# Kernel optimization log

Measured on AMD Instinct MI355X. Metric: run time of the kernel, lower is better.

The kernel has to match this reference:

```python
import jax, jax.numpy as jnp
import numpy as np

EMB = 1024
HEADS = 16
HD = EMB // HEADS

def setup_inputs() -> dict:
    key = jax.random.key(0)
    ks = jax.random.split(key, 9)
    s = 1.0 / np.sqrt(EMB)
    x = jax.random.normal(ks[0], (4, 2048, EMB), dtype=jnp.float32)
    Wq = jax.random.uniform(ks[1], (EMB, EMB), jnp.float32, -s, s)
    bq = jax.random.uniform(ks[2], (EMB,), jnp.float32, -s, s)
    Wk = jax.random.uniform(ks[3], (EMB, EMB), jnp.float32, -s, s)
    bk = jax.random.uniform(ks[4], (EMB,), jnp.float32, -s, s)
    Wv = jax.random.uniform(ks[5], (EMB, EMB), jnp.float32, -s, s)
    bv = jax.random.uniform(ks[6], (EMB,), jnp.float32, -s, s)
    Wo = jax.random.uniform(ks[7], (EMB, EMB), jnp.float32, -s, s)
    bo = jax.random.uniform(ks[8], (EMB,), jnp.float32, -s, s)
    return {"x": x, "Wq": Wq, "bq": bq, "Wk": Wk, "bk": bk, "Wv": Wv, "bv": bv, "Wo": Wo, "bo": bo}

def reference(x, Wq, bq, Wk, bk, Wv, bv, Wo, bo):
    B, T, C = x.shape
    # projections (torch Linear: y = x @ W^T + b)
    q = (x @ Wq.T + bq).reshape(B, T, HEADS, HD).transpose(0, 2, 1, 3)  # [B,H,T,hd]
    k = (x @ Wk.T + bk).reshape(B, T, HEADS, HD).transpose(0, 2, 1, 3)
    v = (x @ Wv.T + bv).reshape(B, T, HEADS, HD).transpose(0, 2, 1, 3)
    scores = jnp.einsum('bhqd,bhkd->bhqk', q, k) / jnp.sqrt(jnp.float32(HD))
    weights = jax.nn.softmax(scores, axis=-1)
    attn = jnp.einsum('bhqk,bhkd->bhqd', weights, v)
    out = attn.transpose(0, 2, 1, 3).reshape(B, T, C)
    return out @ Wo.T + bo
```

## Files before the change

kernel.cpp:

```cpp
#include <hip/hip_runtime.h>

#define TSEQ  2048
#define BATCH 4
#define NHEAD 16
#define EMB   1024

typedef __attribute__((ext_vector_type(8))) __bf16 bf16x8;
typedef __attribute__((ext_vector_type(4))) __bf16 bf16x4;
typedef __attribute__((ext_vector_type(4))) float  floatx4;
typedef __attribute__((ext_vector_type(2))) unsigned int uint32x2;
typedef __attribute__((ext_vector_type(4))) unsigned int uint32x4;

__device__ __forceinline__ void gload_lds16(const __bf16* g, __bf16* lds_uniform_base) {
  __builtin_amdgcn_global_load_lds(
      (__attribute__((address_space(1))) void*)(g),
      (__attribute__((address_space(3))) void*)(lds_uniform_base),
      16, 0, 0);
}

__global__ __launch_bounds__(256) void cvt_f32_bf16(
    const float* __restrict__ src, __bf16* __restrict__ dst)
{
  const int gid = (blockIdx.x * 256 + threadIdx.x) * 4;
  const float4 v = *(const float4*)(src + gid);
  dst[gid + 0] = (__bf16)v.x;
  dst[gid + 1] = (__bf16)v.y;
  dst[gid + 2] = (__bf16)v.z;
  dst[gid + 3] = (__bf16)v.w;
}

__global__ __launch_bounds__(256) void cvt_w4(
    const float* __restrict__ s0, const float* __restrict__ s1,
    const float* __restrict__ s2, const float* __restrict__ s3,
    __bf16* __restrict__ d0, __bf16* __restrict__ d1,
    __bf16* __restrict__ d2, __bf16* __restrict__ d3)
{
  const int z = blockIdx.z;
  const float* src = (z == 0) ? s0 : (z == 1) ? s1 : (z == 2) ? s2 : s3;
  __bf16*      dst = (z == 0) ? d0 : (z == 1) ? d1 : (z == 2) ? d2 : d3;
  const int gid = (blockIdx.x * 256 + threadIdx.x) * 4;
  const float4 v = *(const float4*)(src + gid);
  dst[gid + 0] = (__bf16)v.x;
  dst[gid + 1] = (__bf16)v.y;
  dst[gid + 2] = (__bf16)v.z;
  dst[gid + 3] = (__bf16)v.w;
}

__global__ __launch_bounds__(256) void gemm_bt_bias(
    const __bf16* __restrict__ A,
    const __bf16* __restrict__ W0, const __bf16* __restrict__ W1, const __bf16* __restrict__ W2,
    const float* __restrict__ B0, const float* __restrict__ B1, const float* __restrict__ B2,
    __bf16* __restrict__ C0, __bf16* __restrict__ C1, __bf16* __restrict__ C2)
{
  const int z = blockIdx.z;
  const __bf16* W  = (z == 0) ? W0 : ((z == 1) ? W1 : W2);
  const float*  Bb = (z == 0) ? B0 : ((z == 1) ? B1 : B2);
  __bf16*       C  = (z == 0) ? C0 : ((z == 1) ? C1 : C2);
  const float  scl = (z == 0) ? 0.125f * 1.44269504088896340736f : 1.0f;

  const int tid  = threadIdx.x;
  const int lane = tid & 63;
  const int wid  = tid >> 6;
  const int l16  = lane & 15;
  const int quad = lane >> 4;
  const int wm   = wid & 1;
  const int wn   = wid >> 1;
  const int lin = blockIdx.x + blockIdx.y * 8;
  const int swz = (lin & 7) * 64 + (lin >> 3);
  const int m0  = (swz >> 3) * 128;
  const int n0  = (swz & 7) * 128;

  __shared__ alignas(16) __bf16 As[128 * 32];
  __shared__ alignas(16) __bf16 Bs[128 * 32];

  floatx4 acc[4][4];
#pragma unroll
  for (int i = 0; i < 4; i++)
#pragma unroll
    for (int j = 0; j < 4; j++) acc[i][j] = (floatx4){0.f, 0.f, 0.f, 0.f};

  const int srow = tid >> 2;
  const int sseg = tid & 3;

  for (int k0 = 0; k0 < 1024; k0 += 32) {
    __syncthreads();
#pragma unroll
    for (int is = 0; is < 2; is++) {
      const int row = is * 64 + srow;
      gload_lds16(A + (size_t)(m0 + row) * 1024 + k0 + sseg * 8,
                  &As[(is * 256 + wid * 64) * 8]);
      gload_lds16(W + (size_t)(n0 + row) * 1024 + k0 + sseg * 8,
                  &Bs[(is * 256 + wid * 64) * 8]);
    }
    __syncthreads();

    bf16x8 af[4], bfr[4];
#pragma unroll
    for (int i = 0; i < 4; i++) {
      af[i]  = *(const bf16x8*)(&As[(wm * 64 + i * 16 + l16) * 32 + quad * 8]);
      bfr[i] = *(const bf16x8*)(&Bs[(wn * 64 + i * 16 + l16) * 32 + quad * 8]);
    }
#pragma unroll
    for (int i = 0; i < 4; i++)
#pragma unroll
      for (int j = 0; j < 4; j++)
        acc[i][j] = __builtin_amdgcn_mfma_f32_16x16x32_bf16(af[i], bfr[j], acc[i][j], 0, 0, 0);
  }

  float bv[4];
#pragma unroll
  for (int j = 0; j < 4; j++) bv[j] = Bb[n0 + wn * 64 + j * 16 + l16];

#pragma unroll
  for (int i = 0; i < 4; i++) {
    const size_t mrow = (size_t)m0 + wm * 64 + i * 16 + quad * 4;
#pragma unroll
    for (int j = 0; j < 4; j++) {
      const int col = n0 + wn * 64 + j * 16 + l16;
#pragma unroll
      for (int r = 0; r < 4; r++)
        C[(mrow + r) * 1024 + col] = (__bf16)((acc[i][j][r] + bv[j]) * scl);
    }
  }
}

__global__ __launch_bounds__(256) void gemm_bt_bias_f32(
    const __bf16* __restrict__ A, const __bf16* __restrict__ W,
    const float* __restrict__ Bb, float* __restrict__ C)
{
  const int tid  = threadIdx.x;
  const int lane = tid & 63;
  const int wid  = tid >> 6;
  const int l16  = lane & 15;
  const int quad = lane >> 4;
  const int wm   = wid & 1;
  const int wn   = wid >> 1;
  const int lin = blockIdx.x + blockIdx.y * 8;
  const int swz = (lin & 7) * 64 + (lin >> 3);
  const int m0  = (swz >> 3) * 128;
  const int n0  = (swz & 7) * 128;

  __shared__ alignas(16) __bf16 As[128 * 32];
  __shared__ alignas(16) __bf16 Bs[128 * 32];

  floatx4 acc[4][4];
#pragma unroll
  for (int i = 0; i < 4; i++)
#pragma unroll
    for (int j = 0; j < 4; j++) acc[i][j] = (floatx4){0.f, 0.f, 0.f, 0.f};

  const int srow = tid >> 2;
  const int sseg = tid & 3;

  for (int k0 = 0; k0 < 1024; k0 += 32) {
    __syncthreads();
#pragma unroll
    for (int is = 0; is < 2; is++) {
      const int row = is * 64 + srow;
      gload_lds16(A + (size_t)(m0 + row) * 1024 + k0 + sseg * 8,
                  &As[(is * 256 + wid * 64) * 8]);
      gload_lds16(W + (size_t)(n0 + row) * 1024 + k0 + sseg * 8,
                  &Bs[(is * 256 + wid * 64) * 8]);
    }
    __syncthreads();

    bf16x8 af[4], bfr[4];
#pragma unroll
    for (int i = 0; i < 4; i++) {
      af[i]  = *(const bf16x8*)(&As[(wm * 64 + i * 16 + l16) * 32 + quad * 8]);
      bfr[i] = *(const bf16x8*)(&Bs[(wn * 64 + i * 16 + l16) * 32 + quad * 8]);
    }
#pragma unroll
    for (int i = 0; i < 4; i++)
#pragma unroll
      for (int j = 0; j < 4; j++)
        acc[i][j] = __builtin_amdgcn_mfma_f32_16x16x32_bf16(af[i], bfr[j], acc[i][j], 0, 0, 0);
  }

  float bv[4];
#pragma unroll
  for (int j = 0; j < 4; j++) bv[j] = Bb[n0 + wn * 64 + j * 16 + l16];

#pragma unroll
  for (int i = 0; i < 4; i++) {
    const size_t mrow = (size_t)m0 + wm * 64 + i * 16 + quad * 4;
#pragma unroll
    for (int j = 0; j < 4; j++) {
      const int col = n0 + wn * 64 + j * 16 + l16;
#pragma unroll
      for (int r = 0; r < 4; r++)
        C[(mrow + r) * 1024 + col] = acc[i][j][r] + bv[j];
    }
  }
}

__global__ __launch_bounds__(256) void v_transpose(
    const __bf16* __restrict__ V, __bf16* __restrict__ VT)
{
  const int t0 = blockIdx.x * 64;
  const int bh = blockIdx.y;
  const int b  = bh >> 4;
  const int h  = bh & 15;
  const int tid = threadIdx.x;

  __shared__ alignas(16) __bf16 Ls[64 * 72];

  const int row = tid >> 2, seg = tid & 3;
  const __bf16* src = V + ((size_t)(b * TSEQ + t0 + row)) * EMB + h * 64;
  *(bf16x8*)(&Ls[row * 72 + seg * 8])       = *(const bf16x8*)(src + seg * 8);
  *(bf16x8*)(&Ls[row * 72 + (seg + 4) * 8]) = *(const bf16x8*)(src + (seg + 4) * 8);
  __syncthreads();

  const int od = tid >> 2, oseg = tid & 3;
  bf16x8 o0, o1;
#pragma unroll
  for (int j = 0; j < 8; j++) o0[j] = Ls[(oseg * 16 + j) * 72 + od];
#pragma unroll
  for (int j = 0; j < 8; j++) o1[j] = Ls[(oseg * 16 + 8 + j) * 72 + od];
  __bf16* dst = VT + ((size_t)bh * 64 + od) * TSEQ + t0 + oseg * 16;
  *(bf16x8*)(dst)     = o0;
  *(bf16x8*)(dst + 8) = o1;
}

#define KVB 64
#define NT  (TSEQ / KVB)

#define FA_STEP(BUF, KT)                                                                  \
  {                                                                                       \
    if ((KT) + 1 < NT) {                                                                  \
      *(bf16x8*)(&Ks[(BUF) ^ 1][soff])            = kv0;                                  \
      *(bf16x8*)(&Ks[(BUF) ^ 1][soff + 32 * 72])  = kv1;                                  \
      *(bf16x8*)(&VTs[(BUF) ^ 1][soff])           = vv0;                                  \
      *(bf16x8*)(&VTs[(BUF) ^ 1][soff + 32 * 72]) = vv1;                                  \
    }                                                                                     \
    if ((KT) + 2 < NT) {                                                                  \
      kv0 = *(const bf16x8*)(ksrc + (size_t)(((KT) + 2) * KVB) * EMB);                    \
      kv1 = *(const bf16x8*)(ksrc + (size_t)(((KT) + 2) * KVB + 32) * EMB);               \
      vv0 = *(const bf16x8*)(vsrc + ((KT) + 2) * KVB);                                    \
      vv1 = *(const bf16x8*)(vsrc + (size_t)32 * TSEQ + ((KT) + 2) * KVB);                \
    }                                                                                     \
    __builtin_amdgcn_s_setprio(1);                                                        \
    bf16x8 pfrag[2][2];                                                                   \
    _Pragma("unroll")                                                                     \
    for (int ks = 0; ks < 2; ks++) {                                                      \
      const bf16x8 ka0 = *(const bf16x8*)(&Ks[BUF][((2 * ks) * 16 + l16) * 72 + quad * 8]);      \
      const bf16x8 ka1 = *(const bf16x8*)(&Ks[BUF][((2 * ks) * 16 + l16) * 72 + 32 + quad * 8]); \
      const bf16x8 kb0 = *(const bf16x8*)(&Ks[BUF][((2 * ks + 1) * 16 + l16) * 72 + quad * 8]);  \
      const bf16x8 kb1 = *(const bf16x8*)(&Ks[BUF][((2 * ks + 1) * 16 + l16) * 72 + 32 + quad * 8]); \
      _Pragma("unroll")                                                                   \
      for (int g = 0; g < 2; g++) {                                                       \
        floatx4 ta = (floatx4){0.f, 0.f, 0.f, 0.f};                                       \
        floatx4 tb = (floatx4){0.f, 0.f, 0.f, 0.f};                                       \
        ta = __builtin_amdgcn_mfma_f32_16x16x32_bf16(ka0, qf[g][0], ta, 0, 0, 0);         \
        ta = __builtin_amdgcn_mfma_f32_16x16x32_bf16(ka1, qf[g][1], ta, 0, 0, 0);         \
        tb = __builtin_amdgcn_mfma_f32_16x16x32_bf16(kb0, qf[g][0], tb, 0, 0, 0);         \
        tb = __builtin_amdgcn_mfma_f32_16x16x32_bf16(kb1, qf[g][1], tb, 0, 0, 0);         \
        bf16x4 pa, pb;                                                                    \
        _Pragma("unroll")                                                                 \
        for (int r = 0; r < 4; r++) pa[r] = (__bf16)__builtin_amdgcn_exp2f(ta[r]);        \
        _Pragma("unroll")                                                                 \
        for (int r = 0; r < 4; r++) pb[r] = (__bf16)__builtin_amdgcn_exp2f(tb[r]);        \
        const uint32x2 A2 = __builtin_bit_cast(uint32x2, pa);                             \
        const uint32x2 B2 = __builtin_bit_cast(uint32x2, pb);                             \
        const uint32x2 r0 = __builtin_amdgcn_permlane32_swap(A2.x, B2.x, false, false);   \
        const uint32x2 r1 = __builtin_amdgcn_permlane32_swap(A2.y, B2.y, false, false);   \
        const uint32x2 s0 = __builtin_amdgcn_permlane16_swap(r0.x, r0.y, false, false);   \
        const uint32x2 s1 = __builtin_amdgcn_permlane16_swap(r1.x, r1.y, false, false);   \
        const uint32x4 fw = (uint32x4){s0.x, s1.x, s0.y, s1.y};                           \
        pfrag[g][ks] = __builtin_bit_cast(bf16x8, fw);                                    \
      }                                                                                   \
    }                                                                                     \
    _Pragma("unroll")                                                                     \
    for (int g = 0; g < 2; g++) {                                                         \
      lacc[g] = __builtin_amdgcn_mfma_f32_16x16x32_bf16(ones, pfrag[g][0], lacc[g], 0, 0, 0); \
      lacc[g] = __builtin_amdgcn_mfma_f32_16x16x32_bf16(ones, pfrag[g][1], lacc[g], 0, 0, 0); \
    }                                                                                     \
    _Pragma("unroll")                                                                     \
    for (int dg = 0; dg < 4; dg++) {                                                      \
      _Pragma("unroll")                                                                   \
      for (int ks = 0; ks < 2; ks++) {                                                    \
        const bf16x8 vf = *(const bf16x8*)(&VTs[BUF][(dg * 16 + l16) * 72 + ks * 32 + quad * 8]); \
        _Pragma("unroll")                                                                 \
        for (int g = 0; g < 2; g++)                                                       \
          Oacc[g][dg] = __builtin_amdgcn_mfma_f32_16x16x32_bf16(vf, pfrag[g][ks], Oacc[g][dg], 0, 0, 0); \
      }                                                                                   \
    }                                                                                     \
    __builtin_amdgcn_s_setprio(0);                                                        \
    __syncthreads();                                                                      \
  }

__global__ __launch_bounds__(256, 4) void flash_attn(
    const __bf16* __restrict__ Q, const __bf16* __restrict__ K,
    const __bf16* __restrict__ VT, __bf16* __restrict__ O)
{
  const int lin = blockIdx.x + blockIdx.y * 16;
  const int swz = (lin & 7) * 128 + (lin >> 3);
  const int qt  = swz & 15;
  const int bh  = swz >> 4;
  const int b    = bh >> 4;
  const int h    = bh & 15;
  const int tid  = threadIdx.x;
  const int wid  = tid >> 6;
  const int lane = tid & 63;
  const int l16  = lane & 15;
  const int quad = lane >> 4;

  __shared__ alignas(16) __bf16 Ks[2][KVB * 72];
  __shared__ alignas(16) __bf16 VTs[2][64 * 72];

  const size_t base = ((size_t)b * TSEQ) * EMB + (size_t)h * 64;
  const __bf16* qptr  = Q + base;
  const __bf16* kptr  = K + base;
  const __bf16* vtptr = VT + (size_t)bh * 64 * TSEQ;
  __bf16*       optr  = O + base;

  const int qb = qt * 128 + wid * 32;

  bf16x8 qf[2][2];
#pragma unroll
  for (int g = 0; g < 2; g++)
#pragma unroll
    for (int hf = 0; hf < 2; hf++)
      qf[g][hf] = *(const bf16x8*)(qptr + (size_t)(qb + g * 16 + l16) * EMB + hf * 32 + quad * 8);

  floatx4 Oacc[2][4];
#pragma unroll
  for (int g = 0; g < 2; g++)
#pragma unroll
    for (int dg = 0; dg < 4; dg++) Oacc[g][dg] = (floatx4){0.f, 0.f, 0.f, 0.f};
  floatx4 lacc[2];
#pragma unroll
  for (int g = 0; g < 2; g++) lacc[g] = (floatx4){0.f, 0.f, 0.f, 0.f};

  const uint32x4 onesw = (uint32x4){0x3F803F80u, 0x3F803F80u, 0x3F803F80u, 0x3F803F80u};
  const bf16x8 ones = __builtin_bit_cast(bf16x8, onesw);

  const int srow = tid >> 3, sseg = tid & 7;
  const __bf16* ksrc = kptr  + (size_t)srow * EMB  + sseg * 8;
  const __bf16* vsrc = vtptr + (size_t)srow * TSEQ + sseg * 8;
  const int soff = srow * 72 + sseg * 8;

  bf16x8 kv0 = *(const bf16x8*)(ksrc);
  bf16x8 kv1 = *(const bf16x8*)(ksrc + (size_t)32 * EMB);
  bf16x8 vv0 = *(const bf16x8*)(vsrc);
  bf16x8 vv1 = *(const bf16x8*)(vsrc + (size_t)32 * TSEQ);
  *(bf16x8*)(&Ks[0][soff])            = kv0;
  *(bf16x8*)(&Ks[0][soff + 32 * 72])  = kv1;
  *(bf16x8*)(&VTs[0][soff])           = vv0;
  *(bf16x8*)(&VTs[0][soff + 32 * 72]) = vv1;
  kv0 = *(const bf16x8*)(ksrc + (size_t)KVB * EMB);
  kv1 = *(const bf16x8*)(ksrc + (size_t)(KVB + 32) * EMB);
  vv0 = *(const bf16x8*)(vsrc + KVB);
  vv1 = *(const bf16x8*)(vsrc + (size_t)32 * TSEQ + KVB);
  __syncthreads();

#pragma unroll 1
  for (int kt = 0; kt < NT; kt += 2) {
    FA_STEP(0, kt);
    FA_STEP(1, kt + 1);
  }

#pragma unroll
  for (int g = 0; g < 2; g++) {
    const float inv = 1.0f / lacc[g][0];
#pragma unroll
    for (int dg = 0; dg < 4; dg++) {
      bf16x4 ov;
#pragma unroll
      for (int r = 0; r < 4; r++) ov[r] = (__bf16)(Oacc[g][dg][r] * inv);
      *(bf16x4*)(optr + (size_t)(qb + g * 16 + l16) * EMB + dg * 16 + quad * 4) = ov;
    }
  }
}

extern "C" void kernel_launch(void* const* d_in, const int* in_sizes, int n_in,
                              void* d_out, int out_size, void* d_ws, size_t ws_size,
                              hipStream_t stream) {
  const float* x  = (const float*)d_in[0];
  const float* Wq = (const float*)d_in[1];
  const float* bq = (const float*)d_in[2];
  const float* Wk = (const float*)d_in[3];
  const float* bk = (const float*)d_in[4];
  const float* Wv = (const float*)d_in[5];
  const float* bv = (const float*)d_in[6];
  const float* Wo = (const float*)d_in[7];
  const float* bo = (const float*)d_in[8];
  float* out = (float*)d_out;

  const size_t NELEM = (size_t)BATCH * TSEQ * EMB;
  const size_t WELEM = (size_t)EMB * EMB;

  __bf16* q_b  = (__bf16*)d_out;
  __bf16* k_b  = q_b + NELEM;
  __bf16* x_b  = (__bf16*)d_ws;
  __bf16* v_b  = x_b + NELEM;
  __bf16* wq_b = v_b + NELEM;
  __bf16* wk_b = wq_b + WELEM;
  __bf16* wv_b = wk_b + WELEM;
  __bf16* wo_b = wv_b + WELEM;

  dim3 blk(256, 1, 1);

  cvt_f32_bf16<<<(int)(NELEM / 1024), blk, 0, stream>>>(x, x_b);
  cvt_w4<<<dim3((int)(WELEM / 1024), 1, 4), blk, 0, stream>>>(
      Wq, Wk, Wv, Wo, wq_b, wk_b, wv_b, wo_b);

  gemm_bt_bias<<<dim3(8, 64, 3), blk, 0, stream>>>(
      x_b, wq_b, wk_b, wv_b, bq, bk, bv, q_b, k_b, v_b);

  v_transpose<<<dim3(TSEQ / 64, BATCH * NHEAD), blk, 0, stream>>>(v_b, x_b);

  flash_attn<<<dim3(TSEQ / 128, BATCH * NHEAD), blk, 0, stream>>>(
      q_b, k_b, x_b, v_b);

  gemm_bt_bias_f32<<<dim3(8, 64, 1), blk, 0, stream>>>(v_b, wo_b, bo, out);
}
```

Before: 274.1 us.

## Stage flash-attn K/V via direct global-to-LDS loads with XOR swizzle, 256-row Q tiles

Replaces the register-staged K/V prefetch in the attention kernel with asynchronous global_load_lds copies into unpadded, XOR-swizzled shared memory, so no VGPRs are spent holding the next tile. Each wave now handles 64 query rows instead of 32, doubling K/V reuse per LDS load and halving the grid, with launch bounds lowered to allow more registers. The costs are higher register pressure, lower occupancy, and fewer blocks to balance across CUs. The next tile is also now issued only one step ahead rather than two.

After: 265.3 us. -3.2%, faster.

```diff
diff --git a/kernel.cpp b/kernel.cpp
--- a/kernel.cpp
+++ b/kernel.cpp
@@ -225,30 +225,30 @@
 #define KVB 64
 #define NT  (TSEQ / KVB)
 
+#define FA_STAGE(BUF, TILE)                                                               \
+  if ((TILE) < NT) {                                                                      \
+    _Pragma("unroll")                                                                     \
+    for (int c = 0; c < 2; c++) {                                                         \
+      gload_lds16(kstage + (size_t)((TILE) * KVB + c * 8) * EMB,                          \
+                  &Ks[BUF][(wid * 16 + c * 8) * 64]);                                     \
+      gload_lds16(vstage + (size_t)(c * 8) * TSEQ + (TILE) * KVB,                         \
+                  &VTs[BUF][(wid * 16 + c * 8) * 64]);                                    \
+    }                                                                                     \
+  }
+
 #define FA_STEP(BUF, KT)                                                                  \
   {                                                                                       \
-    if ((KT) + 1 < NT) {                                                                  \
-      *(bf16x8*)(&Ks[(BUF) ^ 1][soff])            = kv0;                                  \
-      *(bf16x8*)(&Ks[(BUF) ^ 1][soff + 32 * 72])  = kv1;                                  \
-      *(bf16x8*)(&VTs[(BUF) ^ 1][soff])           = vv0;                                  \
-      *(bf16x8*)(&VTs[(BUF) ^ 1][soff + 32 * 72]) = vv1;                                  \
-    }                                                                                     \
-    if ((KT) + 2 < NT) {                                                                  \
-      kv0 = *(const bf16x8*)(ksrc + (size_t)(((KT) + 2) * KVB) * EMB);                    \
-      kv1 = *(const bf16x8*)(ksrc + (size_t)(((KT) + 2) * KVB + 32) * EMB);               \
-      vv0 = *(const bf16x8*)(vsrc + ((KT) + 2) * KVB);                                    \
-      vv1 = *(const bf16x8*)(vsrc + (size_t)32 * TSEQ + ((KT) + 2) * KVB);                \
-    }                                                                                     \
+    FA_STAGE((BUF) ^ 1, (KT) + 1);                                                        \
     __builtin_amdgcn_s_setprio(1);                                                        \
-    bf16x8 pfrag[2][2];                                                                   \
+    bf16x8 pfrag[4][2];                                                                   \
     _Pragma("unroll")                                                                     \
     for (int ks = 0; ks < 2; ks++) {                                                      \
-      const bf16x8 ka0 = *(const bf16x8*)(&Ks[BUF][((2 * ks) * 16 + l16) * 72 + quad * 8]);      \
-      const bf16x8 ka1 = *(const bf16x8*)(&Ks[BUF][((2 * ks) * 16 + l16) * 72 + 32 + quad * 8]); \
-      const bf16x8 kb0 = *(const bf16x8*)(&Ks[BUF][((2 * ks + 1) * 16 + l16) * 72 + quad * 8]);  \
-      const bf16x8 kb1 = *(const bf16x8*)(&Ks[BUF][((2 * ks + 1) * 16 + l16) * 72 + 32 + quad * 8]); \
+      const bf16x8 ka0 = *(const bf16x8*)(&Ks[BUF][ks * 2048 + aoff0]);                   \
+      const bf16x8 ka1 = *(const bf16x8*)(&Ks[BUF][ks * 2048 + aoff1]);                   \
+      const bf16x8 kb0 = *(const bf16x8*)(&Ks[BUF][ks * 2048 + 1024 + aoff0]);            \
+      const bf16x8 kb1 = *(const bf16x8*)(&Ks[BUF][ks * 2048 + 1024 + aoff1]);            \
       _Pragma("unroll")                                                                   \
-      for (int g = 0; g < 2; g++) {                                                       \
+      for (int g = 0; g < 4; g++) {                                                       \
         floatx4 ta = (floatx4){0.f, 0.f, 0.f, 0.f};                                       \
         floatx4 tb = (floatx4){0.f, 0.f, 0.f, 0.f};                                       \
         ta = __builtin_amdgcn_mfma_f32_16x16x32_bf16(ka0, qf[g][0], ta, 0, 0, 0);         \
@@ -271,7 +271,7 @@
       }                                                                                   \
     }                                                                                     \
     _Pragma("unroll")                                                                     \
-    for (int g = 0; g < 2; g++) {                                                         \
+    for (int g = 0; g < 4; g++) {                                                         \
       lacc[g] = __builtin_amdgcn_mfma_f32_16x16x32_bf16(ones, pfrag[g][0], lacc[g], 0, 0, 0); \
       lacc[g] = __builtin_amdgcn_mfma_f32_16x16x32_bf16(ones, pfrag[g][1], lacc[g], 0, 0, 0); \
     }                                                                                     \
@@ -279,9 +279,9 @@
     for (int dg = 0; dg < 4; dg++) {                                                      \
       _Pragma("unroll")                                                                   \
       for (int ks = 0; ks < 2; ks++) {                                                    \
-        const bf16x8 vf = *(const bf16x8*)(&VTs[BUF][(dg * 16 + l16) * 72 + ks * 32 + quad * 8]); \
+        const bf16x8 vf = *(const bf16x8*)(&VTs[BUF][dg * 1024 + (ks ? aoff1 : aoff0)]);  \
         _Pragma("unroll")                                                                 \
-        for (int g = 0; g < 2; g++)                                                       \
+        for (int g = 0; g < 4; g++)                                                       \
           Oacc[g][dg] = __builtin_amdgcn_mfma_f32_16x16x32_bf16(vf, pfrag[g][ks], Oacc[g][dg], 0, 0, 0); \
       }                                                                                   \
     }                                                                                     \
@@ -289,14 +289,14 @@
     __syncthreads();                                                                      \
   }
 
-__global__ __launch_bounds__(256, 4) void flash_attn(
+__global__ __launch_bounds__(256, 2) void flash_attn(
     const __bf16* __restrict__ Q, const __bf16* __restrict__ K,
     const __bf16* __restrict__ VT, __bf16* __restrict__ O)
 {
-  const int lin = blockIdx.x + blockIdx.y * 16;
-  const int swz = (lin & 7) * 128 + (lin >> 3);
-  const int qt  = swz & 15;
-  const int bh  = swz >> 4;
+  const int lin = blockIdx.x + blockIdx.y * 8;
+  const int swz = (lin & 7) * 64 + (lin >> 3);
+  const int qt  = swz & 7;
+  const int bh  = swz >> 3;
   const int b    = bh >> 4;
   const int h    = bh & 15;
   const int tid  = threadIdx.x;
@@ -305,8 +305,8 @@
   const int l16  = lane & 15;
   const int quad = lane >> 4;
 
-  __shared__ alignas(16) __bf16 Ks[2][KVB * 72];
-  __shared__ alignas(16) __bf16 VTs[2][64 * 72];
+  __shared__ alignas(16) __bf16 Ks[2][KVB * 64];
+  __shared__ alignas(16) __bf16 VTs[2][64 * 64];
 
   const size_t base = ((size_t)b * TSEQ) * EMB + (size_t)h * 64;
   const __bf16* qptr  = Q + base;
@@ -314,44 +314,38 @@
   const __bf16* vtptr = VT + (size_t)bh * 64 * TSEQ;
   __bf16*       optr  = O + base;
 
-  const int qb = qt * 128 + wid * 32;
-
-  bf16x8 qf[2][2];
-#pragma unroll
-  for (int g = 0; g < 2; g++)
+  const int qb = qt * 256 + wid * 64;
+
+  bf16x8 qf[4][2];
+#pragma unroll
+  for (int g = 0; g < 4; g++)
 #pragma unroll
     for (int hf = 0; hf < 2; hf++)
       qf[g][hf] = *(const bf16x8*)(qptr + (size_t)(qb + g * 16 + l16) * EMB + hf * 32 + quad * 8);
 
-  floatx4 Oacc[2][4];
-#pragma unroll
-  for (int g = 0; g < 2; g++)
+  floatx4 Oacc[4][4];
+#pragma unroll
+  for (int g = 0; g < 4; g++)
 #pragma unroll
     for (int dg = 0; dg < 4; dg++) Oacc[g][dg] = (floatx4){0.f, 0.f, 0.f, 0.f};
-  floatx4 lacc[2];
-#pragma unroll
-  for (int g = 0; g < 2; g++) lacc[g] = (floatx4){0.f, 0.f, 0.f, 0.f};
+  floatx4 lacc[4];
+#pragma unroll
+  for (int g = 0; g < 4; g++) lacc[g] = (floatx4){0.f, 0.f, 0.f, 0.f};
 
   const uint32x4 onesw = (uint32x4){0x3F803F80u, 0x3F803F80u, 0x3F803F80u, 0x3F803F80u};
   const bf16x8 ones = __builtin_bit_cast(bf16x8, onesw);
 
-  const int srow = tid >> 3, sseg = tid & 7;
-  const __bf16* ksrc = kptr  + (size_t)srow * EMB  + sseg * 8;
-  const __bf16* vsrc = vtptr + (size_t)srow * TSEQ + sseg * 8;
-  const int soff = srow * 72 + sseg * 8;
-
-  bf16x8 kv0 = *(const bf16x8*)(ksrc);
-  bf16x8 kv1 = *(const bf16x8*)(ksrc + (size_t)32 * EMB);
-  bf16x8 vv0 = *(const bf16x8*)(vsrc);
-  bf16x8 vv1 = *(const bf16x8*)(vsrc + (size_t)32 * TSEQ);
-  *(bf16x8*)(&Ks[0][soff])            = kv0;
-  *(bf16x8*)(&Ks[0][soff + 32 * 72])  = kv1;
-  *(bf16x8*)(&VTs[0][soff])           = vv0;
-  *(bf16x8*)(&VTs[0][soff + 32 * 72]) = vv1;
-  kv0 = *(const bf16x8*)(ksrc + (size_t)KVB * EMB);
-  kv1 = *(const bf16x8*)(ksrc + (size_t)(KVB + 32) * EMB);
-  vv0 = *(const bf16x8*)(vsrc + KVB);
-  vv1 = *(const bf16x8*)(vsrc + (size_t)32 * TSEQ + KVB);
+  const int lrow = lane >> 3;
+  const int xsg  = (lane & 7) ^ lrow;
+  const __bf16* kstage = kptr  + (size_t)(wid * 16 + lrow) * EMB  + xsg * 8;
+  const __bf16* vstage = vtptr + (size_t)(wid * 16 + lrow) * TSEQ + xsg * 8;
+
+  const int h7    = l16 & 7;
+  const int x0    = quad ^ h7;
+  const int aoff0 = l16 * 64 + x0 * 8;
+  const int aoff1 = l16 * 64 + (x0 ^ 4) * 8;
+
+  FA_STAGE(0, 0);
   __syncthreads();
 
 #pragma unroll 1
@@ -361,7 +355,7 @@
   }
 
 #pragma unroll
-  for (int g = 0; g < 2; g++) {
+  for (int g = 0; g < 4; g++) {
     const float inv = 1.0f / lacc[g][0];
 #pragma unroll
     for (int dg = 0; dg < 4; dg++) {
@@ -410,7 +404,7 @@
 
   v_transpose<<<dim3(TSEQ / 64, BATCH * NHEAD), blk, 0, stream>>>(v_b, x_b);
 
-  flash_attn<<<dim3(TSEQ / 128, BATCH * NHEAD), blk, 0, stream>>>(
+  flash_attn<<<dim3(TSEQ / 256, BATCH * NHEAD), blk, 0, stream>>>(
       q_b, k_b, x_b, v_b);
 
   gemm_bt_bias_f32<<<dim3(8, 64, 1), blk, 0, stream>>>(v_b, wo_b, bo, out);
```
